# Optimization experiments

Hardware: AMD Instinct MI355X
Metric: run time of the kernel (lower is better)

The kernel has to match this reference:

```python
import jax, jax.numpy as jnp
import numpy as np
from jax import lax

D_MODEL = 512
N_STATE = 64
L = 1024
NC = 4  # n_components
HIDDEN = 2 * D_MODEL  # ChannelMix mult=2
R = D_MODEL // 8      # SE reduction
EPS = 1e-5


def hippo_A(N):
    n = np.arange(N, dtype=np.float32)
    t = 2.0 * n + 1.0
    sq = np.sqrt(t[:, None] * t[None, :])
    A = -np.tril(sq, -1) - np.diag(n + 1.0)
    return jnp.asarray(A, jnp.float32)


def setup_inputs() -> dict:
    key = jax.random.key(0)
    ks = jax.random.split(key, 12)
    d, N = D_MODEL, N_STATE
    n = np.arange(N, dtype=np.float32)
    Bref = jnp.asarray(np.sqrt(2.0 * n + 1.0), jnp.float32)
    Bp = jnp.tile(Bref[None, None, :], (NC, d, 1)) + 0.01 * jax.random.normal(ks[0], (NC, d, N))
    Cp = 0.1 * jax.random.normal(ks[1], (NC, d, N))
    Dp = jnp.zeros((NC, d))
    log_dt = jnp.log(0.1 * (1.5 ** jnp.arange(NC, dtype=jnp.float32)))
    x = jax.random.normal(ks[2], (8, L, d))
    s = 0.02
    return {
        "x": x,
        "Bp": Bp, "Cp": Cp, "Dp": Dp, "log_dt": log_dt,
        "se_w1": s * jax.random.normal(ks[3], (R, d)), "se_b1": jnp.zeros((R,)),
        "se_w2": s * jax.random.normal(ks[4], (d, R)), "se_b2": jnp.zeros((d,)),
        "n1_g": jnp.ones((d,)), "n1_b": jnp.zeros((d,)),
        "up_w": s * jax.random.normal(ks[5], (2 * HIDDEN, d)), "up_b": jnp.zeros((2 * HIDDEN,)),
        "down_w": s * jax.random.normal(ks[6], (d, HIDDEN)), "down_b": jnp.zeros((d,)),
        "mixn_g": jnp.ones((d,)), "mixn_b": jnp.zeros((d,)),
        "n2_g": jnp.ones((d,)), "n2_b": jnp.zeros((d,)),
    }


def _ln(x, g, b):
    m = jnp.mean(x, axis=-1, keepdims=True)
    v = jnp.mean(jnp.square(x - m), axis=-1, keepdims=True)
    return (x - m) * lax.rsqrt(v + EPS) * g + b


def _mixture_kernel(Bp, Cp, Dp, log_dt):
    A = hippo_A(N_STATE)
    I = jnp.eye(N_STATE, dtype=jnp.float32)

    def one(Bc, Cc, Dc, ldt):
        dt = jax.nn.softplus(ldt) + 1e-6
        lhs = I - 0.5 * dt * A
        rhs = I + 0.5 * dt * A
        A_bar = jnp.linalg.solve(lhs, rhs)          # (N,N)
        B_bar = jnp.linalg.solve(lhs, (dt * Bc).T).T  # (d,N)

        def step(xs, _):
            y = jnp.einsum('dn,dn->d', Cc, xs)
            return xs @ A_bar.T, y

        _, ys = lax.scan(step, B_bar, None, length=L)  # (L,d)
        K = ys.T  # (d,L)
        return K.at[:, 0].add(Dc)

    return jax.vmap(one)(Bp, Cp, Dp, log_dt).sum(0)  # (d,L)


def reference(x, Bp, Cp, Dp, log_dt,
              se_w1, se_b1, se_w2, se_b2,
              n1_g, n1_b, up_w, up_b, down_w, down_b,
              mixn_g, mixn_b, n2_g, n2_b):
    d = D_MODEL
    K = _mixture_kernel(Bp, Cp, Dp, log_dt)  # (d,L)

    # causal full-length depthwise conv1d
    x_dw = jnp.transpose(x, (0, 2, 1))  # (B,C,T)
    x_pad = jnp.pad(x_dw, ((0, 0), (0, 0), (L - 1, 0)))
    y = lax.conv_general_dilated(
        x_pad, K[:, None, :], window_strides=(1,), padding='VALID',
        feature_group_count=d, dimension_numbers=('NCH', 'OIH', 'NCH'))
    y = jnp.transpose(y, (0, 2, 1))  # (B,T,C)

    # SE gate (squeeze over time)
    s = jnp.mean(y, axis=1)  # (B,C)
    h = jax.nn.relu(s @ se_w1.T + se_b1)
    g = jax.nn.sigmoid(h @ se_w2.T + se_b2)
    y = y * g[:, None, :]

    y1 = _ln(x + y, n1_g, n1_b)

    # ChannelMix (GLU MLP) with residual + LN
    u = y1 @ up_w.T + up_b
    a, gg = jnp.split(u, 2, axis=-1)
    z = (jax.nn.gelu(a, approximate=False) * jax.nn.sigmoid(gg)) @ down_w.T + down_b
    z = _ln(y1 + z, mixn_g, mixn_b)

    return _ln(y1 + z, n2_g, n2_b)
```

## Files before the change

### kernel.cpp

```cpp
#include <hip/hip_runtime.h>
#include <math.h>


typedef short bf16x8 __attribute__((ext_vector_type(8)));
typedef float f32x4 __attribute__((ext_vector_type(4)));

__device__ __forceinline__ float sigmoidf_(float x) { return 1.0f / (1.0f + expf(-x)); }
__device__ __forceinline__ float geluf_(float x) { return 0.5f * x * (1.0f + erff(x * 0.70710678118654752f)); }
__device__ __forceinline__ unsigned short f2bf(float f) {
    unsigned u = __float_as_uint(f);
    unsigned r = (u + 0x7FFFu + ((u >> 16) & 1u)) >> 16;
    return (unsigned short)r;
}
__device__ __forceinline__ unsigned pk2(unsigned short a, unsigned short b) {
    return (unsigned)a | ((unsigned)b << 16);
}
__device__ __forceinline__ void gload16(const void* g, void* l) {
    __builtin_amdgcn_global_load_lds((const __attribute__((address_space(1))) unsigned int*)g,
                                     (__attribute__((address_space(3))) unsigned int*)l, 16, 0, 0);
}

__global__ __launch_bounds__(256) void prep_comp(const float* __restrict__ log_dt,
                                                 float* __restrict__ Pow,
                                                 float* __restrict__ dtbuf) {
    int comp = blockIdx.x, tid = threadIdx.x;
    __shared__ __align__(16) float M1[4096];
    __shared__ __align__(16) float M1T[4096];
    __shared__ __align__(16) float M2[4096];
    __shared__ __align__(16) float M2T[4096];
    float ldt = log_dt[comp];
    float dt = log1pf(expf(ldt)) + 1e-6f;
    float hdt = 0.5f * dt;
    if (tid < 64) {
        int j = tid;
        float sqj = sqrtf(2.0f * (float)j + 1.0f);
        float S = 0.0f;
        for (int i = 0; i < 64; ++i) {
            float sqi = sqrtf(2.0f * (float)i + 1.0f);
            float r = (i == j) ? (1.0f - hdt * (float)(i + 1))
                               : ((i > j) ? (-hdt * sqi * sqj) : 0.0f);
            float X = (r - hdt * sqi * S) / (1.0f + hdt * (float)(i + 1));
            M1[i * 64 + j] = X;
            M1T[j * 64 + i] = X;
            S += sqi * X;
        }
    }
    __syncthreads();
    for (int ii = tid; ii < 4096; ii += 256) Pow[(size_t)comp * 40960 + ii] = M1[ii];
    float* cur = M1; float* curT = M1T; float* nxt = M2; float* nxtT = M2T;
    int ti = tid >> 4, tj = tid & 15;
    for (int s = 1; s <= 9; ++s) {
        float c[4][4] = {{0}};
#pragma unroll 8
        for (int k = 0; k < 64; ++k) {
            float4 a = *(const float4*)&curT[k * 64 + ti * 4];
            float4 b = *(const float4*)&cur[k * 64 + tj * 4];
            c[0][0] += a.x * b.x; c[0][1] += a.x * b.y; c[0][2] += a.x * b.z; c[0][3] += a.x * b.w;
            c[1][0] += a.y * b.x; c[1][1] += a.y * b.y; c[1][2] += a.y * b.z; c[1][3] += a.y * b.w;
            c[2][0] += a.z * b.x; c[2][1] += a.z * b.y; c[2][2] += a.z * b.z; c[2][3] += a.z * b.w;
            c[3][0] += a.w * b.x; c[3][1] += a.w * b.y; c[3][2] += a.w * b.z; c[3][3] += a.w * b.w;
        }
#pragma unroll
        for (int r = 0; r < 4; ++r) {
            float4 row; row.x = c[r][0]; row.y = c[r][1]; row.z = c[r][2]; row.w = c[r][3];
            *(float4*)&nxt[(ti * 4 + r) * 64 + tj * 4] = row;
            float4 colv; colv.x = c[0][r]; colv.y = c[1][r]; colv.z = c[2][r]; colv.w = c[3][r];
            *(float4*)&nxtT[(tj * 4 + r) * 64 + ti * 4] = colv;
        }
        __syncthreads();
        for (int ii = tid; ii < 4096; ii += 256) Pow[(size_t)comp * 40960 + s * 4096 + ii] = nxt[ii];
        float* t0 = cur; cur = nxt; nxt = t0;
        float* t1 = curT; curT = nxtT; nxtT = t1;
        __syncthreads();
    }
    if (tid == 0) dtbuf[comp] = dt;
}

__global__ __launch_bounds__(256) void compute_bbar(const float* __restrict__ Bp,
                                                    const float* __restrict__ dtbuf,
                                                    unsigned short* __restrict__ Bb_h,
                                                    unsigned short* __restrict__ Bb_l) {
    int gid = blockIdx.x * 256 + threadIdx.x;
    int comp = gid >> 9;
    float dt = dtbuf[comp];
    float hdt = 0.5f * dt;
    const float* bp = Bp + (size_t)gid * 64;
    unsigned short* oh = Bb_h + (size_t)gid * 64;
    unsigned short* ol = Bb_l + (size_t)gid * 64;
    float S = 0.0f;
    for (int i = 0; i < 64; ++i) {
        float sqi = sqrtf(2.0f * (float)i + 1.0f);
        float y = (dt * bp[i] - hdt * sqi * S) / (1.0f + hdt * (float)(i + 1));
        unsigned short h = f2bf(y);
        oh[i] = h;
        ol[i] = f2bf(y - __uint_as_float((unsigned)h << 16));
        S += sqi * y;
    }
}

__global__ __launch_bounds__(256) void convert_all(const float* __restrict__ up_w,
                                                   const float* __restrict__ dn_w,
                                                   const float* __restrict__ Cp,
                                                   unsigned short* __restrict__ up_wb,
                                                   unsigned short* __restrict__ dn_wb,
                                                   unsigned short* __restrict__ Cp_h,
                                                   unsigned short* __restrict__ Cp_l) {
    int i = blockIdx.x * 256 + threadIdx.x;
    if (i < 196608) {
        const float* src = (i < 131072) ? up_w : dn_w;
        unsigned short* dst = (i < 131072) ? up_wb : dn_wb;
        int j = (i < 131072) ? i : (i - 131072);
        float4 a = ((const float4*)src)[2 * j];
        float4 b = ((const float4*)src)[2 * j + 1];
        uint4 o;
        o.x = pk2(f2bf(a.x), f2bf(a.y));
        o.y = pk2(f2bf(a.z), f2bf(a.w));
        o.z = pk2(f2bf(b.x), f2bf(b.y));
        o.w = pk2(f2bf(b.z), f2bf(b.w));
        *(uint4*)&dst[(size_t)j * 8] = o;
    } else if (i < 212992) {
        int j = i - 196608;
        float4 a = ((const float4*)Cp)[2 * j];
        float4 b = ((const float4*)Cp)[2 * j + 1];
        float vv[8] = {a.x, a.y, a.z, a.w, b.x, b.y, b.z, b.w};
        unsigned short hs[8], ls[8];
#pragma unroll
        for (int k = 0; k < 8; ++k) {
            unsigned short h = f2bf(vv[k]);
            hs[k] = h;
            ls[k] = f2bf(vv[k] - __uint_as_float((unsigned)h << 16));
        }
        uint4 ho, lo;
        ho.x = pk2(hs[0], hs[1]); ho.y = pk2(hs[2], hs[3]); ho.z = pk2(hs[4], hs[5]); ho.w = pk2(hs[6], hs[7]);
        lo.x = pk2(ls[0], ls[1]); lo.y = pk2(ls[2], ls[3]); lo.z = pk2(ls[4], ls[5]); lo.w = pk2(ls[6], ls[7]);
        *(uint4*)&Cp_h[(size_t)j * 8] = ho;
        *(uint4*)&Cp_l[(size_t)j * 8] = lo;
    }
}

__global__ __launch_bounds__(256) void power_mats(const float* __restrict__ Pow,
                                                  unsigned short* __restrict__ Pst_h,
                                                  unsigned short* __restrict__ Pst_l,
                                                  unsigned short* __restrict__ Qst_h,
                                                  unsigned short* __restrict__ Qst_l) {
    int idx = blockIdx.x, comp = blockIdx.y, tid = threadIdx.x;
    __shared__ __align__(16) float R[4096], RT[4096], R2[4096], R2T[4096], SbT[4096];
    int isP = (idx < 32) ? 1 : 0;
    int f = isP ? idx : (idx - 32);
    int base_s = isP ? 0 : 5;
    const float* PowC = Pow + (size_t)comp * 40960;
    int i_ = tid & 63, kc = (tid >> 6) * 16;
    float* cur = R; float* curT = RT; float* nx = R2; float* nxT = R2T;
    if (f == 0) {
        for (int ii = tid; ii < 4096; ii += 256) {
            float v = ((ii >> 6) == (ii & 63)) ? 1.0f : 0.0f;
            R[ii] = v; RT[ii] = v;
        }
        __syncthreads();
    } else {
        int b0 = __ffs(f) - 1;
        const float* S0 = PowC + (size_t)(base_s + b0) * 4096;
#pragma unroll
        for (int j = 0; j < 16; j += 4) {
            float4 v = *(const float4*)&S0[i_ * 64 + kc + j];
            *(float4*)&R[i_ * 64 + kc + j] = v;
            RT[(kc + j + 0) * 64 + i_] = v.x;
            RT[(kc + j + 1) * 64 + i_] = v.y;
            RT[(kc + j + 2) * 64 + i_] = v.z;
            RT[(kc + j + 3) * 64 + i_] = v.w;
        }
        int rem = f & ~(1 << b0);
        int ti = tid >> 4, tj = tid & 15;
        __syncthreads();
        while (rem) {
            int b = __ffs(rem) - 1; rem &= rem - 1;
            const float* Sb = PowC + (size_t)(base_s + b) * 4096;
#pragma unroll
            for (int j = 0; j < 16; j += 4) {
                float4 v = *(const float4*)&Sb[i_ * 64 + kc + j];
                SbT[(kc + j + 0) * 64 + i_] = v.x;
                SbT[(kc + j + 1) * 64 + i_] = v.y;
                SbT[(kc + j + 2) * 64 + i_] = v.z;
                SbT[(kc + j + 3) * 64 + i_] = v.w;
            }
            __syncthreads();
            float c[4][4] = {{0}};
#pragma unroll 8
            for (int k = 0; k < 64; ++k) {
                float4 a = *(const float4*)&SbT[k * 64 + ti * 4];
                float4 b4 = *(const float4*)&cur[k * 64 + tj * 4];
                c[0][0] += a.x * b4.x; c[0][1] += a.x * b4.y; c[0][2] += a.x * b4.z; c[0][3] += a.x * b4.w;
                c[1][0] += a.y * b4.x; c[1][1] += a.y * b4.y; c[1][2] += a.y * b4.z; c[1][3] += a.y * b4.w;
                c[2][0] += a.z * b4.x; c[2][1] += a.z * b4.y; c[2][2] += a.z * b4.z; c[2][3] += a.z * b4.w;
                c[3][0] += a.w * b4.x; c[3][1] += a.w * b4.y; c[3][2] += a.w * b4.z; c[3][3] += a.w * b4.w;
            }
#pragma unroll
            for (int r = 0; r < 4; ++r) {
                float4 row; row.x = c[r][0]; row.y = c[r][1]; row.z = c[r][2]; row.w = c[r][3];
                *(float4*)&nx[(ti * 4 + r) * 64 + tj * 4] = row;
                float4 colv; colv.x = c[0][r]; colv.y = c[1][r]; colv.z = c[2][r]; colv.w = c[3][r];
                *(float4*)&nxT[(tj * 4 + r) * 64 + ti * 4] = colv;
            }
            __syncthreads();
            float* t0 = cur; cur = nx; nx = t0;
            float* t1 = curT; curT = nxT; nxT = t1;
        }
    }
    const float* src = isP ? cur : curT;
    int outrow = isP ? idx : (idx - 32);
    unsigned short* dh = (isP ? Pst_h : Qst_h) + (size_t)comp * 131072 + (size_t)outrow * 4096;
    unsigned short* dl = (isP ? Pst_l : Qst_l) + (size_t)comp * 131072 + (size_t)outrow * 4096;
    for (int ii = tid * 8; ii < 4096; ii += 2048) {
        float4 v0 = *(const float4*)&src[ii];
        float4 v1 = *(const float4*)&src[ii + 4];
        float vv[8] = {v0.x, v0.y, v0.z, v0.w, v1.x, v1.y, v1.z, v1.w};
        unsigned short hs[8], ls[8];
#pragma unroll
        for (int j = 0; j < 8; ++j) {
            unsigned short h = f2bf(vv[j]);
            hs[j] = h;
            ls[j] = f2bf(vv[j] - __uint_as_float((unsigned)h << 16));
        }
        uint4 ho, lo;
        ho.x = pk2(hs[0], hs[1]); ho.y = pk2(hs[2], hs[3]); ho.z = pk2(hs[4], hs[5]); ho.w = pk2(hs[6], hs[7]);
        lo.x = pk2(ls[0], ls[1]); lo.y = pk2(ls[2], ls[3]); lo.z = pk2(ls[4], ls[5]); lo.w = pk2(ls[6], ls[7]);
        *(uint4*)&dh[ii] = ho;
        *(uint4*)&dl[ii] = lo;
    }
}

__global__ __launch_bounds__(256) void kgemm_uv2(const unsigned short* __restrict__ Bb_h,
                                                 const unsigned short* __restrict__ Bb_l,
                                                 const unsigned short* __restrict__ Pst_h,
                                                 const unsigned short* __restrict__ Pst_l,
                                                 const unsigned short* __restrict__ Cp_h,
                                                 const unsigned short* __restrict__ Cp_l,
                                                 const unsigned short* __restrict__ Qst_h,
                                                 const unsigned short* __restrict__ Qst_l,
                                                 unsigned short* __restrict__ V_h,
                                                 unsigned short* __restrict__ V_l,
                                                 unsigned short* __restrict__ U_h,
                                                 unsigned short* __restrict__ U_l) {
    int zz = blockIdx.z;
    int isV = (zz < 4) ? 1 : 0;
    int comp = isV ? zz : (zz - 4);
    const unsigned short* Ah = isV ? Bb_h : Cp_h;
    const unsigned short* Al = isV ? Bb_l : Cp_l;
    const unsigned short* Bh = isV ? Pst_h : Qst_h;
    const unsigned short* Bl = isV ? Pst_l : Qst_l;
    unsigned short* Ch = isV ? V_h : U_h;
    unsigned short* Cl = isV ? V_l : U_l;
    int m0 = blockIdx.x * 128, n0 = blockIdx.y * 64;
    int tid = threadIdx.x, w = tid >> 6, l = tid & 63;
    __shared__ __align__(16) short Ash[8192], Asl[8192], Bsh[4096], Bsl[4096];
    const unsigned short* Abh = Ah + (size_t)comp * 32768;
    const unsigned short* Abl = Al + (size_t)comp * 32768;
    const unsigned short* Bbh = Bh + (size_t)comp * 131072;
    const unsigned short* Bbl = Bl + (size_t)comp * 131072;
#pragma unroll
    for (int i = 0; i < 4; ++i) {
        int cid = tid + 256 * i;
        int row = cid >> 3, slot = cid & 7;
        int goff = (m0 + row) * 64 + slot * 8;
        int loff = row * 64 + (slot ^ (row & 7)) * 8;
        *(uint4*)&Ash[loff] = *(const uint4*)(Abh + goff);
        *(uint4*)&Asl[loff] = *(const uint4*)(Abl + goff);
    }
#pragma unroll
    for (int i = 0; i < 2; ++i) {
        int cid = tid + 256 * i;
        int row = cid >> 3, slot = cid & 7;
        int goff = (n0 + row) * 64 + slot * 8;
        int loff = row * 64 + (slot ^ (row & 7)) * 8;
        *(uint4*)&Bsh[loff] = *(const uint4*)(Bbh + goff);
        *(uint4*)&Bsl[loff] = *(const uint4*)(Bbl + goff);
    }
    __syncthreads();
    int p = l >> 4, lr = l & 15;
    f32x4 acc[2][4];
#pragma unroll
    for (int rt = 0; rt < 2; ++rt)
#pragma unroll
        for (int ct = 0; ct < 4; ++ct) acc[rt][ct] = (f32x4)0.0f;
#pragma unroll
    for (int ks = 0; ks < 2; ++ks) {
        bf16x8 ah2[2], al2[2], bh2[4], bl2[4];
#pragma unroll
        for (int rt = 0; rt < 2; ++rt) {
            int row = w * 32 + rt * 16 + lr;
            int off = row * 64 + ((ks * 4 + p) ^ (row & 7)) * 8;
            ah2[rt] = *(bf16x8*)&Ash[off];
            al2[rt] = *(bf16x8*)&Asl[off];
        }
#pragma unroll
        for (int ct = 0; ct < 4; ++ct) {
            int cr = ct * 16 + lr;
            int off = cr * 64 + ((ks * 4 + p) ^ (cr & 7)) * 8;
            bh2[ct] = *(bf16x8*)&Bsh[off];
            bl2[ct] = *(bf16x8*)&Bsl[off];
        }
#pragma unroll
        for (int rt = 0; rt < 2; ++rt)
#pragma unroll
            for (int ct = 0; ct < 4; ++ct) {
                acc[rt][ct] = __builtin_amdgcn_mfma_f32_16x16x32_bf16(ah2[rt], bh2[ct], acc[rt][ct], 0, 0, 0);
                acc[rt][ct] = __builtin_amdgcn_mfma_f32_16x16x32_bf16(ah2[rt], bl2[ct], acc[rt][ct], 0, 0, 0);
                acc[rt][ct] = __builtin_amdgcn_mfma_f32_16x16x32_bf16(al2[rt], bh2[ct], acc[rt][ct], 0, 0, 0);
            }
    }
#pragma unroll
    for (int rt = 0; rt < 2; ++rt)
#pragma unroll
        for (int ct = 0; ct < 4; ++ct) {
#pragma unroll
            for (int reg = 0; reg < 4; ++reg) {
                int row = m0 + w * 32 + rt * 16 + p * 4 + reg;
                int col = n0 + ct * 16 + lr;
                float v = acc[rt][ct][reg];
                unsigned short h = f2bf(v);
                unsigned short lo2 = f2bf(v - __uint_as_float((unsigned)h << 16));
                size_t o = (size_t)comp * 1048576 + (size_t)row * 2048 + col;
                Ch[o] = h;
                Cl[o] = lo2;
            }
        }
}

__global__ __launch_bounds__(256) void kgemm_kr(const unsigned short* __restrict__ Uh,
                                                const unsigned short* __restrict__ Ul,
                                                const unsigned short* __restrict__ Vh,
                                                const unsigned short* __restrict__ Vl,
                                                const float* __restrict__ Dp,
                                                float* __restrict__ Kr) {
    int tid = threadIdx.x, w = tid >> 6, l = tid & 63;
    int d = blockIdx.x;
    int g = w * 512 + d;
    int p = l >> 4, lr = l & 15;
    __shared__ float ksh[4096];
    const unsigned short* ubh = Uh + (size_t)g * 2048;
    const unsigned short* ubl = Ul + (size_t)g * 2048;
    const unsigned short* vbh = Vh + (size_t)g * 2048;
    const unsigned short* vbl = Vl + (size_t)g * 2048;
    f32x4 acc[2][2];
    acc[0][0] = (f32x4)0.0f; acc[0][1] = (f32x4)0.0f;
    acc[1][0] = (f32x4)0.0f; acc[1][1] = (f32x4)0.0f;
#pragma unroll
    for (int ks = 0; ks < 2; ++ks) {
        bf16x8 uh2[2], ul2[2], vh2[2], vl2[2];
#pragma unroll
        for (int mt = 0; mt < 2; ++mt) {
            int off = (mt * 16 + lr) * 64 + ks * 32 + p * 8;
            uh2[mt] = *(const bf16x8*)(ubh + off);
            ul2[mt] = *(const bf16x8*)(ubl + off);
            vh2[mt] = *(const bf16x8*)(vbh + off);
            vl2[mt] = *(const bf16x8*)(vbl + off);
        }
#pragma unroll
        for (int mt = 0; mt < 2; ++mt)
#pragma unroll
            for (int nt = 0; nt < 2; ++nt) {
                acc[mt][nt] = __builtin_amdgcn_mfma_f32_16x16x32_bf16(uh2[mt], vh2[nt], acc[mt][nt], 0, 0, 0);
                acc[mt][nt] = __builtin_amdgcn_mfma_f32_16x16x32_bf16(uh2[mt], vl2[nt], acc[mt][nt], 0, 0, 0);
                acc[mt][nt] = __builtin_amdgcn_mfma_f32_16x16x32_bf16(ul2[mt], vh2[nt], acc[mt][nt], 0, 0, 0);
            }
    }
#pragma unroll
    for (int mt = 0; mt < 2; ++mt)
#pragma unroll
        for (int nt = 0; nt < 2; ++nt)
#pragma unroll
            for (int reg = 0; reg < 4; ++reg) {
                int q = mt * 16 + p * 4 + reg;
                int r = nt * 16 + lr;
                ksh[w * 1024 + q * 32 + r] = acc[mt][nt][reg];
            }
    __syncthreads();
#pragma unroll
    for (int j = 0; j < 4; ++j) {
        int ll = tid * 4 + j;
        float s = ksh[ll] + ksh[1024 + ll] + ksh[2048 + ll] + ksh[3072 + ll];
        if (ll == 0) s += Dp[d] + Dp[512 + d] + Dp[1024 + d] + Dp[1536 + d];
        Kr[(size_t)d * 1024 + (1023 - ll)] = s;
    }
}

__global__ __launch_bounds__(256) void transpose_bmat(const float* __restrict__ in,
                                                      float* __restrict__ out,
                                                      int R, int C) {
    __shared__ float tile[32][33];
    int r0 = blockIdx.x * 32, c0 = blockIdx.y * 32, b = blockIdx.z;
    int tx = threadIdx.x & 31, ty = threadIdx.x >> 5;
#pragma unroll
    for (int m = 0; m < 4; ++m)
        tile[ty + 8 * m][tx] = in[((size_t)b * R + r0 + ty + 8 * m) * C + c0 + tx];
    __syncthreads();
#pragma unroll
    for (int m = 0; m < 4; ++m)
        out[((size_t)b * C + c0 + ty + 8 * m) * R + r0 + tx] = tile[tx][ty + 8 * m];
}

__global__ __launch_bounds__(256) void conv_mfma(const float* __restrict__ xT,
                                                 const float* __restrict__ Kr,
                                                 float* __restrict__ yT,
                                                 float* __restrict__ ssum) {
    int c = blockIdx.x, tid = threadIdx.x;
    int w = tid >> 6, l = tid & 63;
    __shared__ __align__(16) float krp[1088];
    __shared__ __align__(16) short xh[8512], xl[8512];
    __shared__ __align__(16) short gh[10240], gl[10240];
    __shared__ float ssh[64];

    {
        float4 kv = *(const float4*)&Kr[(size_t)c * 1024 + tid * 4];
        *(float4*)&krp[32 + tid * 4] = kv;
        if (tid < 8) *(float4*)&krp[tid * 4] = make_float4(0, 0, 0, 0);
        else if (tid < 16) *(float4*)&krp[1056 + (tid - 8) * 4] = make_float4(0, 0, 0, 0);
    }
    if (tid < 32) {
        int b = tid >> 2, g = tid & 3;
        uint4 z = {0, 0, 0, 0};
        *(uint4*)&xh[(b * 133 + g) * 8] = z;
    } else if (tid < 64) {
        int t2 = tid - 32; int b = t2 >> 2, g = t2 & 3;
        uint4 z = {0, 0, 0, 0};
        *(uint4*)&xl[(b * 133 + g) * 8] = z;
    }
#pragma unroll
    for (int i = 0; i < 4; ++i) {
        int gid = tid + 256 * i;
        int b = gid >> 7, gt = gid & 127;
        const float* src = &xT[((size_t)(b * 512 + c)) * 1024 + gt * 8];
        float4 v0 = *(const float4*)src;
        float4 v1 = *(const float4*)(src + 4);
        float vv[8] = {v0.x, v0.y, v0.z, v0.w, v1.x, v1.y, v1.z, v1.w};
        unsigned short hsv[8], lsv[8];
#pragma unroll
        for (int j2 = 0; j2 < 8; ++j2) {
            unsigned short h = f2bf(vv[j2]);
            hsv[j2] = h;
            lsv[j2] = f2bf(vv[j2] - __uint_as_float((unsigned)h << 16));
        }
        uint4 hh, ll;
        hh.x = pk2(hsv[0], hsv[1]); hh.y = pk2(hsv[2], hsv[3]);
        hh.z = pk2(hsv[4], hsv[5]); hh.w = pk2(hsv[6], hsv[7]);
        ll.x = pk2(lsv[0], lsv[1]); ll.y = pk2(lsv[2], lsv[3]);
        ll.z = pk2(lsv[4], lsv[5]); ll.w = pk2(lsv[6], lsv[7]);
        int off = (b * 133 + 4 + gt) * 8;
        *(uint4*)&xh[off] = hh;
        *(uint4*)&xl[off] = ll;
    }
    __syncthreads();

    f32x4 acc[4][2];
#pragma unroll
    for (int i = 0; i < 4; ++i) { acc[i][0] = (f32x4)0.0f; acc[i][1] = (f32x4)0.0f; }

    int lr = l & 15, kg4 = l >> 4;
    for (int ch = 0; ch < 4; ++ch) {
        int dq0 = ch * 8;
        {
            int dqloc = tid >> 5, n = tid & 31, dq = dq0 + dqloc;
            int s0 = 32 * dq + n + 1;
            int a0 = s0 & ~3, sh = s0 & 3;
            float ff[36];
#pragma unroll
            for (int i = 0; i < 9; ++i) *(float4*)&ff[i * 4] = *(const float4*)&krp[a0 + i * 4];
            unsigned short hsv[32], lsv[32];
#pragma unroll
            for (int k = 0; k < 32; ++k) {
                int j2 = 31 - k;
                float v = (sh == 0) ? ff[j2] : (sh == 1) ? ff[j2 + 1] : (sh == 2) ? ff[j2 + 2] : ff[j2 + 3];
                unsigned short h = f2bf(v);
                hsv[k] = h;
                lsv[k] = f2bf(v - __uint_as_float((unsigned)h << 16));
            }
            int gbase = (dqloc * 32 + n) * 5 * 8;
#pragma unroll
            for (int kg = 0; kg < 4; ++kg) {
                uint4 hh, ll;
                hh.x = pk2(hsv[8 * kg + 0], hsv[8 * kg + 1]);
                hh.y = pk2(hsv[8 * kg + 2], hsv[8 * kg + 3]);
                hh.z = pk2(hsv[8 * kg + 4], hsv[8 * kg + 5]);
                hh.w = pk2(hsv[8 * kg + 6], hsv[8 * kg + 7]);
                ll.x = pk2(lsv[8 * kg + 0], lsv[8 * kg + 1]);
                ll.y = pk2(lsv[8 * kg + 2], lsv[8 * kg + 3]);
                ll.z = pk2(lsv[8 * kg + 4], lsv[8 * kg + 5]);
                ll.w = pk2(lsv[8 * kg + 6], lsv[8 * kg + 7]);
                *(uint4*)&gh[gbase + kg * 8] = hh;
                *(uint4*)&gl[gbase + kg * 8] = ll;
            }
        }
        __syncthreads();
        for (int dqloc = 0; dqloc < 8; ++dqloc) {
            int dq = dq0 + dqloc;
            bf16x8 bh[2], bl[2];
#pragma unroll
            for (int nf = 0; nf < 2; ++nf) {
                int go = ((dqloc * 32 + nf * 16 + lr) * 5 + kg4) * 8;
                bh[nf] = *(bf16x8*)&gh[go];
                bl[nf] = *(bf16x8*)&gl[go];
            }
#pragma unroll
            for (int ffi = 0; ffi < 4; ++ffi) {
                int F = w + 4 * ffi;
                if (2 * F + 1 < dq) continue;
                int b = lr & 7, qoff = lr >> 3;
                int q = 2 * F + qoff;
                int j = 4 * (q - dq) + kg4 + 4;
                int xo = (b * 133 + j) * 8;
                bf16x8 ah = *(bf16x8*)&xh[xo];
                bf16x8 al = *(bf16x8*)&xl[xo];
#pragma unroll
                for (int nf = 0; nf < 2; ++nf) {
                    acc[ffi][nf] = __builtin_amdgcn_mfma_f32_16x16x32_bf16(ah, bh[nf], acc[ffi][nf], 0, 0, 0);
                    acc[ffi][nf] = __builtin_amdgcn_mfma_f32_16x16x32_bf16(al, bh[nf], acc[ffi][nf], 0, 0, 0);
                    acc[ffi][nf] = __builtin_amdgcn_mfma_f32_16x16x32_bf16(ah, bl[nf], acc[ffi][nf], 0, 0, 0);
                }
            }
        }
        __syncthreads();
    }

    float bsum[4] = {0, 0, 0, 0};
#pragma unroll
    for (int ffi = 0; ffi < 4; ++ffi) {
        int F = w + 4 * ffi;
#pragma unroll
        for (int nf = 0; nf < 2; ++nf) {
#pragma unroll
            for (int reg = 0; reg < 4; ++reg) {
                int mloc = 4 * kg4 + reg;
                int b = mloc & 7;
                int q = 2 * F + (mloc >> 3);
                int t = 32 * q + nf * 16 + lr;
                yT[((size_t)(b * 512 + c)) * 1024 + t] = acc[ffi][nf][reg];
                bsum[reg] += acc[ffi][nf][reg];
            }
        }
    }
#pragma unroll
    for (int off = 1; off < 16; off <<= 1) {
#pragma unroll
        for (int reg = 0; reg < 4; ++reg) bsum[reg] += __shfl_xor(bsum[reg], off, 64);
    }
    if (lr == 0) {
#pragma unroll
        for (int reg = 0; reg < 4; ++reg) ssh[w * 16 + kg4 * 4 + reg] = bsum[reg];
    }
    __syncthreads();
    if (tid < 8) {
        float tot = 0.0f;
        for (int w2 = 0; w2 < 4; ++w2) tot += ssh[w2 * 16 + tid] + ssh[w2 * 16 + 8 + tid];
        ssum[tid * 512 + c] = tot;
    }
}

__global__ __launch_bounds__(256) void se_kernel(const float* __restrict__ ssum,
                                                 const float* __restrict__ w1,
                                                 const float* __restrict__ b1,
                                                 const float* __restrict__ w2,
                                                 const float* __restrict__ b2,
                                                 float* __restrict__ g) {
    int b = blockIdx.x, tid = threadIdx.x;
    __shared__ float s_sh[512];
    __shared__ float part[256];
    __shared__ float h_sh[64];
    for (int c = tid; c < 512; c += 256) s_sh[c] = ssum[b * 512 + c] * (1.0f / 1024.0f);
    __syncthreads();
    int r = tid & 63, seg = tid >> 6;
    float p = 0.0f;
    for (int c = seg * 128; c < seg * 128 + 128; ++c) p += s_sh[c] * w1[r * 512 + c];
    part[tid] = p;
    __syncthreads();
    if (tid < 64) {
        float h = part[tid] + part[tid + 64] + part[tid + 128] + part[tid + 192] + b1[tid];
        h_sh[tid] = fmaxf(h, 0.0f);
    }
    __syncthreads();
    for (int c = tid; c < 512; c += 256) {
        float acc = b2[c];
#pragma unroll 8
        for (int rr = 0; rr < 64; ++rr) acc += h_sh[rr] * w2[c * 64 + rr];
        g[b * 512 + c] = 1.0f / (1.0f + expf(-acc));
    }
}

__global__ __launch_bounds__(128) void fuse1_kernel(const float* __restrict__ x,
                                                    const float* __restrict__ y,
                                                    const float* __restrict__ g,
                                                    const float* __restrict__ n1g,
                                                    const float* __restrict__ n1b,
                                                    unsigned short* __restrict__ y1b) {
    int row = blockIdx.x, b = row >> 10, tid = threadIdx.x, c = tid * 4;
    __shared__ float r1[2], r2[2];
    float4 xv = *(const float4*)&x[(size_t)row * 512 + c];
    float4 yv = *(const float4*)&y[(size_t)row * 512 + c];
    float4 gv = *(const float4*)&g[b * 512 + c];
    float4 v;
    v.x = xv.x + yv.x * gv.x; v.y = xv.y + yv.y * gv.y;
    v.z = xv.z + yv.z * gv.z; v.w = xv.w + yv.w * gv.w;
    float s1 = v.x + v.y + v.z + v.w;
    float s2 = v.x * v.x + v.y * v.y + v.z * v.z + v.w * v.w;
#pragma unroll
    for (int off = 32; off > 0; off >>= 1) {
        s1 += __shfl_down(s1, off, 64);
        s2 += __shfl_down(s2, off, 64);
    }
    if ((tid & 63) == 0) { r1[tid >> 6] = s1; r2[tid >> 6] = s2; }
    __syncthreads();
    float mean = (r1[0] + r1[1]) * (1.0f / 512.0f);
    float var = (r2[0] + r2[1]) * (1.0f / 512.0f) - mean * mean;
    float rstd = rsqrtf(var + 1e-5f);
    float4 g4 = *(const float4*)&n1g[c];
    float4 b4 = *(const float4*)&n1b[c];
    float4 o;
    o.x = (v.x - mean) * rstd * g4.x + b4.x; o.y = (v.y - mean) * rstd * g4.y + b4.y;
    o.z = (v.z - mean) * rstd * g4.z + b4.z; o.w = (v.w - mean) * rstd * g4.w + b4.w;
    uint2 pk;
    pk.x = pk2(f2bf(o.x), f2bf(o.y));
    pk.y = pk2(f2bf(o.z), f2bf(o.w));
    *(uint2*)&y1b[(size_t)row * 512 + c] = pk;
}

__device__ __forceinline__ int swz_slot(int slot, int row) {
    return slot ^ (row & 3) ^ ((row >> 2) & 3);
}

__global__ __launch_bounds__(256) void gemm_glu(const unsigned short* __restrict__ A,
                                                const unsigned short* __restrict__ W,
                                                const float* __restrict__ bias,
                                                unsigned short* __restrict__ act) {
    const int K = 512;
    int m0 = blockIdx.x * 128, n0 = blockIdx.y * 64;
    int tid = threadIdx.x, w = tid >> 6, l = tid & 63;
    __shared__ __align__(16) short As[4096];
    __shared__ __align__(16) short Bs[4096];
    int seg0 = 2 * w, seg1 = 2 * w + 1;
    int rA0 = seg0 * 16 + (l >> 2), rA1 = seg1 * 16 + (l >> 2);
    int ss0 = (l & 3) ^ (rA0 & 3) ^ ((rA0 >> 2) & 3);
    int ss1 = (l & 3) ^ (rA1 & 3) ^ ((rA1 >> 2) & 3);
    const unsigned short* gA0 = A + (size_t)(m0 + rA0) * K + ss0 * 8;
    const unsigned short* gA1 = A + (size_t)(m0 + rA1) * K + ss1 * 8;
    int gBr0 = (rA0 < 64) ? (n0 + rA0) : (1024 + n0 + rA0 - 64);
    int gBr1 = (rA1 < 64) ? (n0 + rA1) : (1024 + n0 + rA1 - 64);
    const unsigned short* gB0 = W + (size_t)gBr0 * K + ss0 * 8;
    const unsigned short* gB1 = W + (size_t)gBr1 * K + ss1 * 8;
    short* ldsA0 = &As[seg0 * 512];
    short* ldsA1 = &As[seg1 * 512];
    short* ldsB0 = &Bs[seg0 * 512];
    short* ldsB1 = &Bs[seg1 * 512];
    int p = l >> 4, lr = l & 15;
    int aoff[2], bAoff[4], bGoff[4];
#pragma unroll
    for (int rt = 0; rt < 2; ++rt) {
        int r = w * 32 + rt * 16 + lr;
        aoff[rt] = r * 32 + swz_slot(p, r) * 8;
    }
#pragma unroll
    for (int ct = 0; ct < 4; ++ct) {
        int ca = ct * 16 + lr, cg = 64 + ct * 16 + lr;
        bAoff[ct] = ca * 32 + swz_slot(p, ca) * 8;
        bGoff[ct] = cg * 32 + swz_slot(p, cg) * 8;
    }
    f32x4 accA[2][4], accG[2][4];
#pragma unroll
    for (int rt = 0; rt < 2; ++rt)
#pragma unroll
        for (int ct = 0; ct < 4; ++ct) {
            accA[rt][ct] = (f32x4)0.0f;
            accG[rt][ct] = (f32x4)0.0f;
        }
    for (int kt = 0; kt < K; kt += 32) {
        __syncthreads();
        gload16(gA0 + kt, ldsA0);
        gload16(gA1 + kt, ldsA1);
        gload16(gB0 + kt, ldsB0);
        gload16(gB1 + kt, ldsB1);
        __syncthreads();
        bf16x8 af[2], bA[4], bG[4];
#pragma unroll
        for (int rt = 0; rt < 2; ++rt) af[rt] = *(bf16x8*)&As[aoff[rt]];
#pragma unroll
        for (int ct = 0; ct < 4; ++ct) {
            bA[ct] = *(bf16x8*)&Bs[bAoff[ct]];
            bG[ct] = *(bf16x8*)&Bs[bGoff[ct]];
        }
#pragma unroll
        for (int rt = 0; rt < 2; ++rt)
#pragma unroll
            for (int ct = 0; ct < 4; ++ct) {
                accA[rt][ct] = __builtin_amdgcn_mfma_f32_16x16x32_bf16(af[rt], bA[ct], accA[rt][ct], 0, 0, 0);
                accG[rt][ct] = __builtin_amdgcn_mfma_f32_16x16x32_bf16(af[rt], bG[ct], accG[rt][ct], 0, 0, 0);
            }
    }
#pragma unroll
    for (int rt = 0; rt < 2; ++rt)
#pragma unroll
        for (int ct = 0; ct < 4; ++ct) {
            int col = n0 + ct * 16 + lr;
            float ba = bias[col], bg = bias[1024 + col];
#pragma unroll
            for (int reg = 0; reg < 4; ++reg) {
                int row = m0 + w * 32 + rt * 16 + p * 4 + reg;
                float a = accA[rt][ct][reg] + ba;
                float g = accG[rt][ct][reg] + bg;
                act[(size_t)row * 1024 + col] = f2bf(geluf_(a) * sigmoidf_(g));
            }
        }
}

__global__ __launch_bounds__(256) void gemm_plain(const unsigned short* __restrict__ A,
                                                  const unsigned short* __restrict__ W,
                                                  const float* __restrict__ bias,
                                                  float* __restrict__ Cout) {
    const int K = 1024, N = 512;
    int m0 = blockIdx.x * 128, n0 = blockIdx.y * 128;
    int tid = threadIdx.x, w = tid >> 6, l = tid & 63;
    int wr = w >> 1, wc = w & 1;
    __shared__ __align__(16) short As[4096];
    __shared__ __align__(16) short Bs[4096];
    int seg0 = 2 * w, seg1 = 2 * w + 1;
    int rA0 = seg0 * 16 + (l >> 2), rA1 = seg1 * 16 + (l >> 2);
    int ss0 = (l & 3) ^ (rA0 & 3) ^ ((rA0 >> 2) & 3);
    int ss1 = (l & 3) ^ (rA1 & 3) ^ ((rA1 >> 2) & 3);
    const unsigned short* gA0 = A + (size_t)(m0 + rA0) * K + ss0 * 8;
    const unsigned short* gA1 = A + (size_t)(m0 + rA1) * K + ss1 * 8;
    const unsigned short* gB0 = W + (size_t)(n0 + rA0) * K + ss0 * 8;
    const unsigned short* gB1 = W + (size_t)(n0 + rA1) * K + ss1 * 8;
    short* ldsA0 = &As[seg0 * 512];
    short* ldsA1 = &As[seg1 * 512];
    short* ldsB0 = &Bs[seg0 * 512];
    short* ldsB1 = &Bs[seg1 * 512];
    int p = l >> 4, lr = l & 15;
    int aoff[4], boff[4];
#pragma unroll
    for (int t = 0; t < 4; ++t) {
        int r = wr * 64 + t * 16 + lr;
        aoff[t] = r * 32 + swz_slot(p, r) * 8;
        int cq = wc * 64 + t * 16 + lr;
        boff[t] = cq * 32 + swz_slot(p, cq) * 8;
    }
    f32x4 acc[4][4];
#pragma unroll
    for (int i = 0; i < 4; ++i)
#pragma unroll
        for (int j = 0; j < 4; ++j) acc[i][j] = (f32x4)0.0f;
    for (int kt = 0; kt < K; kt += 32) {
        __syncthreads();
        gload16(gA0 + kt, ldsA0);
        gload16(gA1 + kt, ldsA1);
        gload16(gB0 + kt, ldsB0);
        gload16(gB1 + kt, ldsB1);
        __syncthreads();
        bf16x8 af[4], bfr[4];
#pragma unroll
        for (int t = 0; t < 4; ++t) {
            af[t] = *(bf16x8*)&As[aoff[t]];
            bfr[t] = *(bf16x8*)&Bs[boff[t]];
        }
#pragma unroll
        for (int i = 0; i < 4; ++i)
#pragma unroll
            for (int j = 0; j < 4; ++j)
                acc[i][j] = __builtin_amdgcn_mfma_f32_16x16x32_bf16(af[i], bfr[j], acc[i][j], 0, 0, 0);
    }
#pragma unroll
    for (int i = 0; i < 4; ++i)
#pragma unroll
        for (int j = 0; j < 4; ++j) {
            int col = n0 + wc * 64 + j * 16 + lr;
            float bb = bias[col];
#pragma unroll
            for (int reg = 0; reg < 4; ++reg) {
                int row = m0 + wr * 64 + i * 16 + p * 4 + reg;
                Cout[(size_t)row * N + col] = acc[i][j][reg] + bb;
            }
        }
}

__global__ __launch_bounds__(128) void fuse2_kernel(const unsigned short* __restrict__ y1b,
                                                    const float* __restrict__ z,
                                                    const float* __restrict__ mg,
                                                    const float* __restrict__ mb,
                                                    const float* __restrict__ g2,
                                                    const float* __restrict__ b2v,
                                                    float* __restrict__ out) {
    int row = blockIdx.x, tid = threadIdx.x, c = tid * 4;
    __shared__ float r1[2], r2[2];
    uint2 yu = *(const uint2*)&y1b[(size_t)row * 512 + c];
    float4 a;
    a.x = __uint_as_float(yu.x << 16);
    a.y = __uint_as_float(yu.x & 0xffff0000u);
    a.z = __uint_as_float(yu.y << 16);
    a.w = __uint_as_float(yu.y & 0xffff0000u);
    float4 zv = *(const float4*)&z[(size_t)row * 512 + c];
    float4 t1;
    t1.x = a.x + zv.x; t1.y = a.y + zv.y; t1.z = a.z + zv.z; t1.w = a.w + zv.w;
    float s1 = t1.x + t1.y + t1.z + t1.w;
    float s2 = t1.x * t1.x + t1.y * t1.y + t1.z * t1.z + t1.w * t1.w;
#pragma unroll
    for (int off = 32; off > 0; off >>= 1) {
        s1 += __shfl_down(s1, off, 64);
        s2 += __shfl_down(s2, off, 64);
    }
    if ((tid & 63) == 0) { r1[tid >> 6] = s1; r2[tid >> 6] = s2; }
    __syncthreads();
    float mean = (r1[0] + r1[1]) * (1.0f / 512.0f);
    float var = (r2[0] + r2[1]) * (1.0f / 512.0f) - mean * mean;
    float rstd = rsqrtf(var + 1e-5f);
    float4 mg4 = *(const float4*)&mg[c];
    float4 mb4 = *(const float4*)&mb[c];
    float4 t2;
    t2.x = a.x + ((t1.x - mean) * rstd * mg4.x + mb4.x);
    t2.y = a.y + ((t1.y - mean) * rstd * mg4.y + mb4.y);
    t2.z = a.z + ((t1.z - mean) * rstd * mg4.z + mb4.z);
    t2.w = a.w + ((t1.w - mean) * rstd * mg4.w + mb4.w);
    __syncthreads();
    s1 = t2.x + t2.y + t2.z + t2.w;
    s2 = t2.x * t2.x + t2.y * t2.y + t2.z * t2.z + t2.w * t2.w;
#pragma unroll
    for (int off = 32; off > 0; off >>= 1) {
        s1 += __shfl_down(s1, off, 64);
        s2 += __shfl_down(s2, off, 64);
    }
    if ((tid & 63) == 0) { r1[tid >> 6] = s1; r2[tid >> 6] = s2; }
    __syncthreads();
    float mean2 = (r1[0] + r1[1]) * (1.0f / 512.0f);
    float var2 = (r2[0] + r2[1]) * (1.0f / 512.0f) - mean2 * mean2;
    float rstd2 = rsqrtf(var2 + 1e-5f);
    float4 gg = *(const float4*)&g2[c];
    float4 bb = *(const float4*)&b2v[c];
    float4 o;
    o.x = (t2.x - mean2) * rstd2 * gg.x + bb.x;
    o.y = (t2.y - mean2) * rstd2 * gg.y + bb.y;
    o.z = (t2.z - mean2) * rstd2 * gg.z + bb.z;
    o.w = (t2.w - mean2) * rstd2 * gg.w + bb.w;
    *(float4*)&out[(size_t)row * 512 + c] = o;
}

extern "C" void kernel_launch(void* const* d_in, const int* in_sizes, int n_in,
                              void* d_out, int out_size, void* d_ws, size_t ws_size,
                              hipStream_t stream) {
    (void)in_sizes; (void)n_in; (void)out_size; (void)ws_size;
    const float* x      = (const float*)d_in[0];
    const float* Bp     = (const float*)d_in[1];
    const float* Cp     = (const float*)d_in[2];
    const float* Dp     = (const float*)d_in[3];
    const float* log_dt = (const float*)d_in[4];
    const float* se_w1  = (const float*)d_in[5];
    const float* se_b1  = (const float*)d_in[6];
    const float* se_w2  = (const float*)d_in[7];
    const float* se_b2  = (const float*)d_in[8];
    const float* n1g    = (const float*)d_in[9];
    const float* n1b    = (const float*)d_in[10];
    const float* up_w   = (const float*)d_in[11];
    const float* up_b   = (const float*)d_in[12];
    const float* dn_w   = (const float*)d_in[13];
    const float* dn_b   = (const float*)d_in[14];
    const float* mxg    = (const float*)d_in[15];
    const float* mxb    = (const float*)d_in[16];
    const float* n2g    = (const float*)d_in[17];
    const float* n2b    = (const float*)d_in[18];

    float* ws = (float*)d_ws;
    float* Kr   = ws + 0;
    float* dtb  = ws + 524288;
    float* ssum = ws + 524352;
    float* gbuf = ws + 528448;
    unsigned short* up_wb = (unsigned short*)(ws + 532544);
    unsigned short* dn_wb = (unsigned short*)(ws + 1056832);
    float* Pow  = ws + 1450048;
    unsigned short* Bb_h = (unsigned short*)(ws + 1613888);
    unsigned short* Bb_l = (unsigned short*)(ws + 1679424);
    unsigned short* Cp_h = (unsigned short*)(ws + 1744960);
    unsigned short* Cp_l = (unsigned short*)(ws + 1810496);
    unsigned short* Pst_h = (unsigned short*)(ws + 1876032);
    unsigned short* Pst_l = (unsigned short*)(ws + 2138176);
    unsigned short* Qst_h = (unsigned short*)(ws + 2400320);
    unsigned short* Qst_l = (unsigned short*)(ws + 2662464);
    unsigned short* U_h = (unsigned short*)(ws + 5021760);
    unsigned short* U_l = (unsigned short*)(ws + 7118912);
    unsigned short* V_h = (unsigned short*)(ws + 9216064);
    unsigned short* V_l = (unsigned short*)(ws + 11313216);
    float* xT   = ws + 5021760;
    float* yT   = ws + 9216064;
    float* yb   = ws + 13410368;
    unsigned short* y1b = (unsigned short*)(ws + 9216064);
    unsigned short* act = (unsigned short*)(ws + 5021760);
    float* zb   = ws + 13410368;
    float* outp = (float*)d_out;

    hipLaunchKernelGGL(prep_comp, dim3(4), dim3(256), 0, stream, log_dt, Pow, dtb);
    hipLaunchKernelGGL(compute_bbar, dim3(8), dim3(256), 0, stream, Bp, dtb, Bb_h, Bb_l);
    hipLaunchKernelGGL(convert_all, dim3(832), dim3(256), 0, stream, up_w, dn_w, Cp, up_wb, dn_wb, Cp_h, Cp_l);
    hipLaunchKernelGGL(power_mats, dim3(64, 4), dim3(256), 0, stream, Pow, Pst_h, Pst_l, Qst_h, Qst_l);
    hipLaunchKernelGGL(kgemm_uv2, dim3(4, 32, 8), dim3(256), 0, stream,
                       Bb_h, Bb_l, Pst_h, Pst_l, Cp_h, Cp_l, Qst_h, Qst_l, V_h, V_l, U_h, U_l);
    hipLaunchKernelGGL(kgemm_kr, dim3(512), dim3(256), 0, stream, U_h, U_l, V_h, V_l, Dp, Kr);
    hipLaunchKernelGGL(transpose_bmat, dim3(32, 16, 8), dim3(256), 0, stream, x, xT, 1024, 512);
    hipLaunchKernelGGL(conv_mfma, dim3(512), dim3(256), 0, stream, xT, Kr, yT, ssum);
    hipLaunchKernelGGL(se_kernel, dim3(8), dim3(256), 0, stream, ssum, se_w1, se_b1, se_w2, se_b2, gbuf);
    hipLaunchKernelGGL(transpose_bmat, dim3(16, 32, 8), dim3(256), 0, stream, yT, yb, 512, 1024);
    hipLaunchKernelGGL(fuse1_kernel, dim3(8192), dim3(128), 0, stream, x, yb, gbuf, n1g, n1b, y1b);
    hipLaunchKernelGGL(gemm_glu, dim3(64, 16), dim3(256), 0, stream, y1b, up_wb, up_b, act);
    hipLaunchKernelGGL(gemm_plain, dim3(64, 4), dim3(256), 0, stream, act, dn_wb, dn_b, zb);
    hipLaunchKernelGGL(fuse2_kernel, dim3(8192), dim3(128), 0, stream, y1b, zb, mxg, mxb, n2g, n2b, outp);
}
```

Measured before the change: 235.1 us.

## Double-buffer LDS tiles in GLU and down-projection GEMMs

Both bf16 MFMA GEMM kernels now keep two LDS buffers per operand. Each k-step prefetches the next k-tile into the other buffer with global_load_lds while MFMAs run on the current one, which also drops one of the two barriers per iteration. The aim is to hide global-to-LDS load latency behind compute. In exchange, LDS use per block doubles, which may lower occupancy. Correctness also relies on the barrier waiting for the outstanding LDS-direct loads.

```diff
diff --git a/kernel.cpp b/kernel.cpp
--- a/kernel.cpp
+++ b/kernel.cpp
@@ -633,8 +633,8 @@
     const int K = 512;
     int m0 = blockIdx.x * 128, n0 = blockIdx.y * 64;
     int tid = threadIdx.x, w = tid >> 6, l = tid & 63;
-    __shared__ __align__(16) short As[4096];
-    __shared__ __align__(16) short Bs[4096];
+    __shared__ __align__(16) short As[2][4096];
+    __shared__ __align__(16) short Bs[2][4096];
     int seg0 = 2 * w, seg1 = 2 * w + 1;
     int rA0 = seg0 * 16 + (l >> 2), rA1 = seg1 * 16 + (l >> 2);
     int ss0 = (l & 3) ^ (rA0 & 3) ^ ((rA0 >> 2) & 3);
@@ -645,10 +645,6 @@
     int gBr1 = (rA1 < 64) ? (n0 + rA1) : (1024 + n0 + rA1 - 64);
     const unsigned short* gB0 = W + (size_t)gBr0 * K + ss0 * 8;
     const unsigned short* gB1 = W + (size_t)gBr1 * K + ss1 * 8;
-    short* ldsA0 = &As[seg0 * 512];
-    short* ldsA1 = &As[seg1 * 512];
-    short* ldsB0 = &Bs[seg0 * 512];
-    short* ldsB1 = &Bs[seg1 * 512];
     int p = l >> 4, lr = l & 15;
     int aoff[2], bAoff[4], bGoff[4];
 #pragma unroll
@@ -670,20 +666,27 @@
             accA[rt][ct] = (f32x4)0.0f;
             accG[rt][ct] = (f32x4)0.0f;
         }
+    gload16(gA0, &As[0][seg0 * 512]);
+    gload16(gA1, &As[0][seg1 * 512]);
+    gload16(gB0, &Bs[0][seg0 * 512]);
+    gload16(gB1, &Bs[0][seg1 * 512]);
+    int cur = 0;
     for (int kt = 0; kt < K; kt += 32) {
         __syncthreads();
-        gload16(gA0 + kt, ldsA0);
-        gload16(gA1 + kt, ldsA1);
-        gload16(gB0 + kt, ldsB0);
-        gload16(gB1 + kt, ldsB1);
-        __syncthreads();
+        if (kt + 32 < K) {
+            int nb = cur ^ 1;
+            gload16(gA0 + kt + 32, &As[nb][seg0 * 512]);
+            gload16(gA1 + kt + 32, &As[nb][seg1 * 512]);
+            gload16(gB0 + kt + 32, &Bs[nb][seg0 * 512]);
+            gload16(gB1 + kt + 32, &Bs[nb][seg1 * 512]);
+        }
         bf16x8 af[2], bA[4], bG[4];
 #pragma unroll
-        for (int rt = 0; rt < 2; ++rt) af[rt] = *(bf16x8*)&As[aoff[rt]];
+        for (int rt = 0; rt < 2; ++rt) af[rt] = *(bf16x8*)&As[cur][aoff[rt]];
 #pragma unroll
         for (int ct = 0; ct < 4; ++ct) {
-            bA[ct] = *(bf16x8*)&Bs[bAoff[ct]];
-            bG[ct] = *(bf16x8*)&Bs[bGoff[ct]];
+            bA[ct] = *(bf16x8*)&Bs[cur][bAoff[ct]];
+            bG[ct] = *(bf16x8*)&Bs[cur][bGoff[ct]];
         }
 #pragma unroll
         for (int rt = 0; rt < 2; ++rt)
@@ -692,6 +695,7 @@
                 accA[rt][ct] = __builtin_amdgcn_mfma_f32_16x16x32_bf16(af[rt], bA[ct], accA[rt][ct], 0, 0, 0);
                 accG[rt][ct] = __builtin_amdgcn_mfma_f32_16x16x32_bf16(af[rt], bG[ct], accG[rt][ct], 0, 0, 0);
             }
+        cur ^= 1;
     }
 #pragma unroll
     for (int rt = 0; rt < 2; ++rt)
@@ -717,8 +721,8 @@
     int m0 = blockIdx.x * 128, n0 = blockIdx.y * 128;
     int tid = threadIdx.x, w = tid >> 6, l = tid & 63;
     int wr = w >> 1, wc = w & 1;
-    __shared__ __align__(16) short As[4096];
-    __shared__ __align__(16) short Bs[4096];
+    __shared__ __align__(16) short As[2][4096];
+    __shared__ __align__(16) short Bs[2][4096];
     int seg0 = 2 * w, seg1 = 2 * w + 1;
     int rA0 = seg0 * 16 + (l >> 2), rA1 = seg1 * 16 + (l >> 2);
     int ss0 = (l & 3) ^ (rA0 & 3) ^ ((rA0 >> 2) & 3);
@@ -727,10 +731,6 @@
     const unsigned short* gA1 = A + (size_t)(m0 + rA1) * K + ss1 * 8;
     const unsigned short* gB0 = W + (size_t)(n0 + rA0) * K + ss0 * 8;
     const unsigned short* gB1 = W + (size_t)(n0 + rA1) * K + ss1 * 8;
-    short* ldsA0 = &As[seg0 * 512];
-    short* ldsA1 = &As[seg1 * 512];
-    short* ldsB0 = &Bs[seg0 * 512];
-    short* ldsB1 = &Bs[seg1 * 512];
     int p = l >> 4, lr = l & 15;
     int aoff[4], boff[4];
 #pragma unroll
@@ -745,24 +745,32 @@
     for (int i = 0; i < 4; ++i)
 #pragma unroll
         for (int j = 0; j < 4; ++j) acc[i][j] = (f32x4)0.0f;
+    gload16(gA0, &As[0][seg0 * 512]);
+    gload16(gA1, &As[0][seg1 * 512]);
+    gload16(gB0, &Bs[0][seg0 * 512]);
+    gload16(gB1, &Bs[0][seg1 * 512]);
+    int cur = 0;
     for (int kt = 0; kt < K; kt += 32) {
         __syncthreads();
-        gload16(gA0 + kt, ldsA0);
-        gload16(gA1 + kt, ldsA1);
-        gload16(gB0 + kt, ldsB0);
-        gload16(gB1 + kt, ldsB1);
-        __syncthreads();
+        if (kt + 32 < K) {
+            int nb = cur ^ 1;
+            gload16(gA0 + kt + 32, &As[nb][seg0 * 512]);
+            gload16(gA1 + kt + 32, &As[nb][seg1 * 512]);
+            gload16(gB0 + kt + 32, &Bs[nb][seg0 * 512]);
+            gload16(gB1 + kt + 32, &Bs[nb][seg1 * 512]);
+        }
         bf16x8 af[4], bfr[4];
 #pragma unroll
         for (int t = 0; t < 4; ++t) {
-            af[t] = *(bf16x8*)&As[aoff[t]];
-            bfr[t] = *(bf16x8*)&Bs[boff[t]];
+            af[t] = *(bf16x8*)&As[cur][aoff[t]];
+            bfr[t] = *(bf16x8*)&Bs[cur][boff[t]];
         }
 #pragma unroll
         for (int i = 0; i < 4; ++i)
 #pragma unroll
             for (int j = 0; j < 4; ++j)
                 acc[i][j] = __builtin_amdgcn_mfma_f32_16x16x32_bf16(af[i], bfr[j], acc[i][j], 0, 0, 0);
+        cur ^= 1;
     }
 #pragma unroll
     for (int i = 0; i < 4; ++i)
```

New measurement: 234.4 us. No clear change (-0.3%).
